# Performance work log

Measured on AMD Instinct MI355X. Metric: run time of the kernel, lower is better.

The kernel has to match this reference:

```python
import jax, jax.numpy as jnp
import numpy as np

B, S, E, H, HD, RD, MP = 2, 2048, 1024, 16, 64, 32, 8  # batch, seq, embed, heads, head_dim, rotary_dim, mp_num


def rotate_every_two(x):
    # x: [..., D] -> interleave (-x_odd, x_even)
    x1 = x[..., ::2]
    x2 = x[..., 1::2]
    return jnp.stack((-x2, x1), axis=-1).reshape(x.shape)


def apply_rotary(x, sin, cos):
    # x: [B,S,H,RD]; sin/cos: [S, RD//2] -> repeat_interleave(2) -> [1,S,1,RD]
    sin = jnp.repeat(sin, 2, axis=-1)[None, :, None, :]
    cos = jnp.repeat(cos, 2, axis=-1)[None, :, None, :]
    return x * cos + rotate_every_two(x) * sin


def setup_inputs() -> dict:
    key = jax.random.key(0)
    k1, k2, k3 = jax.random.split(key, 3)
    return {
        "hidden_states": jax.random.normal(k1, (B, S, E), dtype=jnp.float32),
        "w_qkv": jax.random.normal(k2, (3 * E, E), dtype=jnp.float32) * 0.02,
        "w_out": jax.random.normal(k3, (E, E), dtype=jnp.float32) * 0.02,
    }


def reference(hidden_states, w_qkv, w_out):
    qkv = hidden_states @ w_qkv.T                      # [B,S,3E]
    local = HD * H // MP                               # 128
    qkv = qkv.reshape(B, S, MP, 3 * local)
    # torch.split order in source is (query, value, key)
    q, v, k = jnp.split(qkv, 3, axis=-1)               # each [B,S,MP,local]

    def split_heads(x):
        return x.reshape(B, S, MP, H // MP, HD).reshape(B, S, H, HD)

    q, k, v = split_heads(q), split_heads(k), split_heads(v)  # [B,S,H,HD]

    # fixed sinusoidal rotary embedding over first RD dims
    inv_freq = 1.0 / 10000 ** (jnp.arange(0, RD, 2, dtype=jnp.float32) / RD)
    sinusoid = jnp.arange(S, dtype=jnp.float32)[:, None] * inv_freq[None, :]  # [S, RD//2]
    sin, cos = jnp.sin(sinusoid), jnp.cos(sinusoid)

    q = jnp.concatenate([apply_rotary(q[..., :RD], sin, cos), q[..., RD:]], axis=-1)
    k = jnp.concatenate([apply_rotary(k[..., :RD], sin, cos), k[..., RD:]], axis=-1)

    # [B,H,S,HD]
    q = q.transpose(0, 2, 1, 3)
    k = k.transpose(0, 2, 1, 3)
    v = v.transpose(0, 2, 1, 3)

    scores = jnp.einsum('bhqd,bhkd->bhqk', q, k) / np.float32(np.sqrt(HD))
    causal = jnp.tril(jnp.ones((S, S), dtype=bool))
    scores = jnp.where(causal[None, None], scores, jnp.float32(-1e9))
    attn = jax.nn.softmax(scores.astype(jnp.float32), axis=-1).astype(q.dtype)
    out = jnp.einsum('bhqk,bhkd->bhqd', attn, v)       # [B,H,S,HD]
    out = out.transpose(0, 2, 1, 3).reshape(B, S, E)
    return out @ w_out.T
```

## Files before the change

kernel.cpp:

```cpp
#include <hip/hip_runtime.h>
#include <hip/hip_bf16.h>

typedef __attribute__((ext_vector_type(8))) short short8;
typedef __attribute__((ext_vector_type(4))) float v4f;

#define ASYNC_COPY16(ldsptr, gptr)                                                        \
  __builtin_amdgcn_global_load_lds((const __attribute__((address_space(1))) void*)(gptr), \
                                   (__attribute__((address_space(3))) void*)(ldsptr),     \
                                   16, 0, 0)

__device__ __forceinline__ unsigned short f2bf(float f) {
  unsigned int u = __float_as_uint(f);
  u += 0x7fffu + ((u >> 16) & 1u);
  return (unsigned short)(u >> 16);
}

__global__ void convert_all(const float* __restrict__ h, const float* __restrict__ wq,
                            const float* __restrict__ wo, unsigned short* __restrict__ ho,
                            unsigned short* __restrict__ wqo, unsigned short* __restrict__ woo) {
  int i = (blockIdx.x * blockDim.x + threadIdx.x) * 4;
  const float* src;
  unsigned short* dst;
  int j;
  if (i < 4194304) { src = h; dst = ho; j = i; }
  else if (i < 7340032) { src = wq; dst = wqo; j = i - 4194304; }
  else { src = wo; dst = woo; j = i - 7340032; }
  float4 v = *(const float4*)(src + j);
  ushort4 o;
  o.x = f2bf(v.x); o.y = f2bf(v.y); o.z = f2bf(v.z); o.w = f2bf(v.w);
  *(ushort4*)(dst + j) = o;
}

#define STAGE_SWZ(tt) ((((tt) & 3) ^ (((tt) >> 3) & 3)) * 8)
#define READ_SWZ(kb, lr) (((kb) ^ (((lr) >> 1) & 3)) * 8)

__global__ __launch_bounds__(256, 6) void gemm_out(const unsigned short* __restrict__ A,
                                                   const unsigned short* __restrict__ Bm,
                                                   float* __restrict__ C, int M, int N, int K) {
  __shared__ __attribute__((aligned(16))) unsigned short As[2 * 64 * 32];
  __shared__ __attribute__((aligned(16))) unsigned short Bs[2 * 64 * 32];
  int t = threadIdx.x;
  int w = t >> 6, lane = t & 63, kb = lane >> 4, lr = lane & 15;
  int m0 = blockIdx.y * 64, n0 = blockIdx.x * 64;
  int wm = (w >> 1) * 32, wn = (w & 1) * 32;
  v4f acc[2][2];
#pragma unroll
  for (int i = 0; i < 2; i++)
#pragma unroll
    for (int j = 0; j < 2; j++) acc[i][j] = (v4f){0.f, 0.f, 0.f, 0.f};
  int ra = m0 + (t >> 2);
  int rb = n0 + (t >> 2);
  int ca = STAGE_SWZ(t);
  int rs = READ_SWZ(kb, lr);
  int nit = K >> 5;
  auto stage = [&](int it, int buf) {
    int base = buf * 2048;
    int k0 = it * 32;
    ASYNC_COPY16(&As[base + t * 8], A + (size_t)ra * K + k0 + ca);
    ASYNC_COPY16(&Bs[base + t * 8], Bm + (size_t)rb * K + k0 + ca);
  };
  stage(0, 0);
  __syncthreads();
  for (int it = 0; it < nit; it++) {
    int cur = (it & 1) * 2048;
    if (it + 1 < nit) stage(it + 1, (it + 1) & 1);
    short8 av[2], bv[2];
#pragma unroll
    for (int i = 0; i < 2; i++) av[i] = *(const short8*)&As[cur + (wm + i * 16 + lr) * 32 + rs];
#pragma unroll
    for (int j = 0; j < 2; j++) bv[j] = *(const short8*)&Bs[cur + (wn + j * 16 + lr) * 32 + rs];
#pragma unroll
    for (int i = 0; i < 2; i++)
#pragma unroll
      for (int j = 0; j < 2; j++)
        acc[i][j] = __builtin_amdgcn_mfma_f32_16x16x32_bf16(av[i], bv[j], acc[i][j], 0, 0, 0);
    __syncthreads();
  }
#pragma unroll
  for (int i = 0; i < 2; i++) {
    int row = m0 + wm + i * 16 + kb * 4;
#pragma unroll
    for (int j = 0; j < 2; j++) {
      int col = n0 + wn + j * 16 + lr;
#pragma unroll
      for (int r = 0; r < 4; r++) C[(size_t)(row + r) * N + col] = acc[i][j][r];
    }
  }
}

__global__ __launch_bounds__(256, 6) void gemm_qkv(const unsigned short* __restrict__ A,
                                                   const unsigned short* __restrict__ Bm,
                                                   unsigned short* __restrict__ Q,
                                                   unsigned short* __restrict__ Ko,
                                                   unsigned short* __restrict__ Vt) {
  constexpr int Kd = 1024;
  __shared__ __attribute__((aligned(16))) unsigned short As[2 * 128 * 32];
  __shared__ __attribute__((aligned(16))) unsigned short Bs[2 * 64 * 32];
  int t = threadIdx.x;
  int w = t >> 6, lane = t & 63, kb = lane >> 4, lr = lane & 15;
  int m0 = blockIdx.y * 128, n0 = blockIdx.x * 64;
  int wm = (w >> 1) * 64, wn = (w & 1) * 32;
  v4f acc[4][2];
#pragma unroll
  for (int i = 0; i < 4; i++)
#pragma unroll
    for (int j = 0; j < 2; j++) acc[i][j] = (v4f){0.f, 0.f, 0.f, 0.f};
  int ra = m0 + (t >> 2);
  int rb = n0 + (t >> 2);
  int ca = STAGE_SWZ(t);
  int rs = READ_SWZ(kb, lr);
  auto stage = [&](int it, int buf) {
    int k0 = it * 32;
    int abase = buf * 4096, bbase = buf * 2048;
    ASYNC_COPY16(&As[abase + t * 8],        A + (size_t)ra * Kd + k0 + ca);
    ASYNC_COPY16(&As[abase + 2048 + t * 8], A + (size_t)(ra + 64) * Kd + k0 + ca);
    ASYNC_COPY16(&Bs[bbase + t * 8],        Bm + (size_t)rb * Kd + k0 + ca);
  };
  stage(0, 0);
  __syncthreads();
  for (int it = 0; it < 32; it++) {
    int acur = (it & 1) * 4096, bcur = (it & 1) * 2048;
    if (it + 1 < 32) stage(it + 1, (it + 1) & 1);
    short8 av[4], bv[2];
#pragma unroll
    for (int i = 0; i < 4; i++)
      av[i] = *(const short8*)&As[acur + (wm + i * 16 + lr) * 32 + rs];
#pragma unroll
    for (int j = 0; j < 2; j++)
      bv[j] = *(const short8*)&Bs[bcur + (wn + j * 16 + lr) * 32 + rs];
#pragma unroll
    for (int i = 0; i < 4; i++)
#pragma unroll
      for (int j = 0; j < 2; j++)
        acc[i][j] = __builtin_amdgcn_mfma_f32_16x16x32_bf16(av[i], bv[j], acc[i][j], 0, 0, 0);
    __syncthreads();
  }
  int X = n0 >> 6;
  int mp = X / 6;
  int sub = X - mp * 6;
  int type = sub >> 1;
  int ii = sub & 1;
  int h = mp * 2 + ii;
  const float qs = 0.125f * 1.4426950408889634f;
  if (type == 1) {
#pragma unroll
    for (int i = 0; i < 4; i++) {
      int row = m0 + wm + i * 16 + kb * 4;
#pragma unroll
      for (int j = 0; j < 2; j++) {
        int dim = wn + j * 16 + lr;
#pragma unroll
        for (int r = 0; r < 4; r++) {
          int m = row + r;
          int b = m >> 11, sl = m & 2047;
          int bh = b * 16 + h;
          int p = (sl & ~31) | ((sl & 15) << 1) | ((sl >> 4) & 1);
          Vt[(size_t)bh * 131072 + (size_t)dim * 2048 + p] = f2bf(acc[i][j][r]);
        }
      }
    }
  } else {
    unsigned short* dst = (type == 0) ? Q : Ko;
    float scale = (type == 0) ? qs : 1.0f;
#pragma unroll
    for (int i = 0; i < 4; i++) {
      int row = m0 + wm + i * 16 + kb * 4;
#pragma unroll
      for (int j = 0; j < 2; j++) {
        int dim = wn + j * 16 + lr;
        float vals[4];
#pragma unroll
        for (int r = 0; r < 4; r++) vals[r] = acc[i][j][r];
        if (dim < 32) {
          int jp = dim >> 1;
          float invf = expf(-(float)jp * 0.57564627324851142f);
#pragma unroll
          for (int r = 0; r < 4; r++) {
            int sl = (row + r) & 2047;
            float ang = (float)sl * invf;
            float sn, cs;
            sincosf(ang, &sn, &cs);
            float partner = __shfl_xor(vals[r], 1);
            float self = vals[r] * cs;
            vals[r] = (lr & 1) ? fmaf(partner, sn, self) : fmaf(-partner, sn, self);
          }
        }
#pragma unroll
        for (int r = 0; r < 4; r++) {
          int m = row + r;
          int b = m >> 11, sl = m & 2047;
          int bh = b * 16 + h;
          dst[(((size_t)(bh * 2048 + sl)) << 6) + dim] = f2bf(vals[r] * scale);
        }
      }
    }
  }
}

__global__ __launch_bounds__(256, 6) void attn_fused(const unsigned short* __restrict__ Qg,
                                                     const unsigned short* __restrict__ Kg,
                                                     const unsigned short* __restrict__ Vtg,
                                                     unsigned short* __restrict__ AO,
                                                     float* __restrict__ PO,
                                                     float* __restrict__ PL) {
  __shared__ __attribute__((aligned(16))) unsigned short Ks[2 * 2048];
  __shared__ __attribute__((aligned(16))) unsigned short Vs[2 * 2048];
  __shared__ __attribute__((aligned(16))) unsigned short Ps[4 * 16 * 40];
  int t = threadIdx.x;
  int w = t >> 6, lane = t & 63, kb = lane >> 4, lr = lane & 15;
  int gid = blockIdx.x;
  int g3 = gid & 7;
  int b2 = (gid >> 3) & 3;
  int z = (gid >> 5) & 7;
  int coset = gid >> 8;
  int bh = g3 * 4 + b2;
  int j = (coset == 0) ? (2 * z)
        : (coset == 1) ? (15 - 2 * z)
        : (coset == 2) ? (16 + z)
        : (coset == 3) ? (31 - z)
        : (coset == 4) ? (32 + z)
                       : (47 - z);
  int qtile, kt0, kt1, mode;
  if (j < 16)      { qtile = j;      mode = 0; kt0 = 0;          kt1 = 2 * qtile + 2; }
  else if (j < 32) { qtile = j;      mode = 1; kt0 = 0;          kt1 = qtile + 1; }
  else             { qtile = j - 16; mode = 2; kt0 = qtile + 1;  kt1 = 2 * qtile + 2; }
  int m0 = qtile * 64;
  const unsigned short* Qb = Qg + (size_t)bh * 2048 * 64;
  const unsigned short* Kb = Kg + (size_t)bh * 2048 * 64;
  const unsigned short* Vb = Vtg + (size_t)bh * 64 * 2048;

  short8 aq0 = *(const short8*)(Qb + (size_t)(m0 + w * 16 + lr) * 64 + kb * 8);
  short8 aq1 = *(const short8*)(Qb + (size_t)(m0 + w * 16 + lr) * 64 + 32 + kb * 8);

  v4f acc[4];
  float lp[4];
#pragma unroll
  for (int n = 0; n < 4; n++) acc[n] = (v4f){0.f, 0.f, 0.f, 0.f};
#pragma unroll
  for (int r = 0; r < 4; r++) lp[r] = 0.f;

  int mrow = w * 16 + kb * 4;

  int kc = t >> 5, krow_s = t & 31;
  int vc = t >> 6, vd = t & 63;
  auto stage = [&](int kt, int buf) {
    int base = buf * 2048;
    ASYNC_COPY16(&Ks[base + t * 8], Kb + (size_t)(kt * 32 + krow_s) * 64 + kc * 8);
    ASYNC_COPY16(&Vs[base + t * 8], Vb + (size_t)vd * 2048 + kt * 32 + vc * 8);
  };

  stage(kt0, 0);
  __syncthreads();

  unsigned short* Pw = &Ps[w * 640];
  int niter = kt1 - kt0;
  for (int it = 0; it < niter; it++) {
    int kt = kt0 + it;
    int cur = (it & 1) * 2048;
    if (it + 1 < niter) stage(kt + 1, (it + 1) & 1);
    v4f sc[2];
#pragma unroll
    for (int n2 = 0; n2 < 2; n2++) {
      int krow = n2 * 16 + lr;
      short8 bk0 = *(const short8*)&Ks[cur + (kb * 32 + krow) * 8];
      short8 bk1 = *(const short8*)&Ks[cur + ((kb + 4) * 32 + krow) * 8];
      v4f zz = (v4f){0.f, 0.f, 0.f, 0.f};
      zz = __builtin_amdgcn_mfma_f32_16x16x32_bf16(aq0, bk0, zz, 0, 0, 0);
      zz = __builtin_amdgcn_mfma_f32_16x16x32_bf16(aq1, bk1, zz, 0, 0, 0);
      sc[n2] = zz;
    }
    if (kt >= 2 * qtile) {
#pragma unroll
      for (int n2 = 0; n2 < 2; n2++)
#pragma unroll
        for (int r = 0; r < 4; r++) {
          int key = kt * 32 + n2 * 16 + lr;
          if (key > m0 + mrow + r) sc[n2][r] = -1e30f;
        }
    }
#pragma unroll
    for (int r = 0; r < 4; r++) {
      float p0 = exp2f(sc[0][r]);
      float p1 = exp2f(sc[1][r]);
      lp[r] += p0 + p1;
      __hip_bfloat162 pb = __float22bfloat162_rn(float2{p0, p1});
      *(__hip_bfloat162*)&Pw[(mrow & 15) * 40 + r * 40 + lr * 2] = pb;
    }
    short8 ap = *(const short8*)&Pw[lr * 40 + kb * 8];
#pragma unroll
    for (int dt = 0; dt < 4; dt++) {
      int d = dt * 16 + lr;
      short8 bv = *(const short8*)&Vs[cur + (kb * 64 + d) * 8];
      acc[dt] = __builtin_amdgcn_mfma_f32_16x16x32_bf16(ap, bv, acc[dt], 0, 0, 0);
    }
    __syncthreads();
  }
  float s[4];
#pragma unroll
  for (int r = 0; r < 4; r++) {
    s[r] = lp[r];
#pragma unroll
    for (int off = 1; off < 16; off <<= 1) s[r] += __shfl_xor(s[r], off);
  }
  if (mode == 0) {
    int b = bh >> 4, h = bh & 15;
#pragma unroll
    for (int r = 0; r < 4; r++) {
      float inv = 1.0f / s[r];
      int qrow = m0 + mrow + r;
#pragma unroll
      for (int dt = 0; dt < 4; dt++)
        AO[(size_t)(b * 2048 + qrow) * 1024 + h * 64 + dt * 16 + lr] = f2bf(acc[dt][r] * inv);
    }
  } else {
    int hf = mode - 1;
    size_t pbase = ((size_t)hf * 512 + bh * 16 + (qtile - 16)) * 4096;
    size_t plbase = (size_t)hf * 32768 + (bh * 16 + (qtile - 16)) * 64;
#pragma unroll
    for (int r = 0; r < 4; r++) {
      if (lr == 0) PL[plbase + mrow + r] = s[r];
#pragma unroll
      for (int dt = 0; dt < 4; dt++)
        PO[pbase + (size_t)(mrow + r) * 64 + dt * 16 + lr] = acc[dt][r];
    }
  }
}

__global__ __launch_bounds__(256) void combine(const float* __restrict__ PO,
                                               const float* __restrict__ PL,
                                               unsigned short* __restrict__ AO) {
  int idx = blockIdx.x * 256 + threadIdx.x;
  int d4 = (idx & 15) * 4;
  int row10 = (idx >> 4) & 1023;
  int bh = idx >> 14;
  int q16 = row10 >> 6, lrow = row10 & 63;
  size_t pbase = (((size_t)(bh * 16 + q16)) * 64 + lrow) * 64 + d4;
  float4 a = *(const float4*)&PO[pbase];
  float4 c = *(const float4*)&PO[2097152 + pbase];
  float l = PL[(bh * 16 + q16) * 64 + lrow] + PL[32768 + (bh * 16 + q16) * 64 + lrow];
  float inv = 1.0f / l;
  ushort4 o;
  o.x = f2bf((a.x + c.x) * inv);
  o.y = f2bf((a.y + c.y) * inv);
  o.z = f2bf((a.z + c.z) * inv);
  o.w = f2bf((a.w + c.w) * inv);
  int b = bh >> 4, h = bh & 15;
  int qrow = 1024 + row10;
  *(ushort4*)&AO[(size_t)(b * 2048 + qrow) * 1024 + h * 64 + d4] = o;
}

extern "C" void kernel_launch(void* const* d_in, const int* in_sizes, int n_in,
                              void* d_out, int out_size, void* d_ws, size_t ws_size,
                              hipStream_t stream) {
  const float* hidden = (const float*)d_in[0];
  const float* w_qkv = (const float*)d_in[1];
  const float* w_out = (const float*)d_in[2];
  float* out = (float*)d_out;
  char* ws = (char*)d_ws;
  unsigned short* hid_bf = (unsigned short*)(ws);
  unsigned short* wqkv_bf = (unsigned short*)(ws + (8ull << 20));
  unsigned short* wout_bf = (unsigned short*)(ws + (14ull << 20));
  unsigned short* Qb = (unsigned short*)(ws + (16ull << 20));
  unsigned short* Kb = (unsigned short*)(ws + (24ull << 20));
  unsigned short* Vt = (unsigned short*)(ws + (32ull << 20));
  unsigned short* AO = (unsigned short*)(ws + (40ull << 20));
  float* PO = (float*)(ws + (48ull << 20));
  float* PL = (float*)(ws + (64ull << 20));

  convert_all<<<8192, 256, 0, stream>>>(hidden, w_qkv, w_out, hid_bf, wqkv_bf, wout_bf);
  gemm_qkv<<<dim3(48, 32), 256, 0, stream>>>(hid_bf, wqkv_bf, Qb, Kb, Vt);
  attn_fused<<<1536, 256, 0, stream>>>(Qb, Kb, Vt, AO, PO, PL);
  combine<<<2048, 256, 0, stream>>>(PO, PL, AO);
  gemm_out<<<dim3(16, 64), 256, 0, stream>>>(AO, wout_bf, out, 4096, 1024, 1024);
}
```

Baseline: 192.9 us.

## Fuse fp32-to-bf16 conversion into GEMMs and split-KV combine into output GEMM

Removes the standalone convert kernel: the QKV and output GEMMs now load fp32 operands into registers, convert them to bf16 and store them to LDS, in a register-prefetch / commit pipeline instead of async global-to-LDS copies. The combine kernel is also folded into the output GEMM, which merges the two partial attention outputs and their normalisers while staging the A tile for rows in the second half of the sequence. This drops two launches and the round trips for the bf16 copies and the combined AO, at the cost of reading fp32 weights repeatedly (twice the bytes per tile), higher register pressure, and conversion work on the GEMM critical path.

```diff
diff --git a/kernel.cpp b/kernel.cpp
--- a/kernel.cpp
+++ b/kernel.cpp
@@ -15,81 +15,17 @@
   return (unsigned short)(u >> 16);
 }
 
-__global__ void convert_all(const float* __restrict__ h, const float* __restrict__ wq,
-                            const float* __restrict__ wo, unsigned short* __restrict__ ho,
-                            unsigned short* __restrict__ wqo, unsigned short* __restrict__ woo) {
-  int i = (blockIdx.x * blockDim.x + threadIdx.x) * 4;
-  const float* src;
-  unsigned short* dst;
-  int j;
-  if (i < 4194304) { src = h; dst = ho; j = i; }
-  else if (i < 7340032) { src = wq; dst = wqo; j = i - 4194304; }
-  else { src = wo; dst = woo; j = i - 7340032; }
-  float4 v = *(const float4*)(src + j);
-  ushort4 o;
-  o.x = f2bf(v.x); o.y = f2bf(v.y); o.z = f2bf(v.z); o.w = f2bf(v.w);
-  *(ushort4*)(dst + j) = o;
-}
-
 #define STAGE_SWZ(tt) ((((tt) & 3) ^ (((tt) >> 3) & 3)) * 8)
 #define READ_SWZ(kb, lr) (((kb) ^ (((lr) >> 1) & 3)) * 8)
 
-__global__ __launch_bounds__(256, 6) void gemm_out(const unsigned short* __restrict__ A,
-                                                   const unsigned short* __restrict__ Bm,
-                                                   float* __restrict__ C, int M, int N, int K) {
-  __shared__ __attribute__((aligned(16))) unsigned short As[2 * 64 * 32];
-  __shared__ __attribute__((aligned(16))) unsigned short Bs[2 * 64 * 32];
-  int t = threadIdx.x;
-  int w = t >> 6, lane = t & 63, kb = lane >> 4, lr = lane & 15;
-  int m0 = blockIdx.y * 64, n0 = blockIdx.x * 64;
-  int wm = (w >> 1) * 32, wn = (w & 1) * 32;
-  v4f acc[2][2];
-#pragma unroll
-  for (int i = 0; i < 2; i++)
-#pragma unroll
-    for (int j = 0; j < 2; j++) acc[i][j] = (v4f){0.f, 0.f, 0.f, 0.f};
-  int ra = m0 + (t >> 2);
-  int rb = n0 + (t >> 2);
-  int ca = STAGE_SWZ(t);
-  int rs = READ_SWZ(kb, lr);
-  int nit = K >> 5;
-  auto stage = [&](int it, int buf) {
-    int base = buf * 2048;
-    int k0 = it * 32;
-    ASYNC_COPY16(&As[base + t * 8], A + (size_t)ra * K + k0 + ca);
-    ASYNC_COPY16(&Bs[base + t * 8], Bm + (size_t)rb * K + k0 + ca);
-  };
-  stage(0, 0);
-  __syncthreads();
-  for (int it = 0; it < nit; it++) {
-    int cur = (it & 1) * 2048;
-    if (it + 1 < nit) stage(it + 1, (it + 1) & 1);
-    short8 av[2], bv[2];
-#pragma unroll
-    for (int i = 0; i < 2; i++) av[i] = *(const short8*)&As[cur + (wm + i * 16 + lr) * 32 + rs];
-#pragma unroll
-    for (int j = 0; j < 2; j++) bv[j] = *(const short8*)&Bs[cur + (wn + j * 16 + lr) * 32 + rs];
-#pragma unroll
-    for (int i = 0; i < 2; i++)
-#pragma unroll
-      for (int j = 0; j < 2; j++)
-        acc[i][j] = __builtin_amdgcn_mfma_f32_16x16x32_bf16(av[i], bv[j], acc[i][j], 0, 0, 0);
-    __syncthreads();
-  }
-#pragma unroll
-  for (int i = 0; i < 2; i++) {
-    int row = m0 + wm + i * 16 + kb * 4;
-#pragma unroll
-    for (int j = 0; j < 2; j++) {
-      int col = n0 + wn + j * 16 + lr;
-#pragma unroll
-      for (int r = 0; r < 4; r++) C[(size_t)(row + r) * N + col] = acc[i][j][r];
-    }
-  }
-}
-
-__global__ __launch_bounds__(256, 6) void gemm_qkv(const unsigned short* __restrict__ A,
-                                                   const unsigned short* __restrict__ Bm,
+__device__ __forceinline__ void cvt_store(unsigned short* dst, float4 f0, float4 f1) {
+  unsigned short v8[8] = {f2bf(f0.x), f2bf(f0.y), f2bf(f0.z), f2bf(f0.w),
+                          f2bf(f1.x), f2bf(f1.y), f2bf(f1.z), f2bf(f1.w)};
+  *(short8*)dst = *(short8*)v8;
+}
+
+__global__ __launch_bounds__(256, 5) void gemm_qkv(const float* __restrict__ A,
+                                                   const float* __restrict__ Bm,
                                                    unsigned short* __restrict__ Q,
                                                    unsigned short* __restrict__ Ko,
                                                    unsigned short* __restrict__ Vt) {
@@ -109,18 +45,31 @@
   int rb = n0 + (t >> 2);
   int ca = STAGE_SWZ(t);
   int rs = READ_SWZ(kb, lr);
-  auto stage = [&](int it, int buf) {
+  float4 pa[4], pb[2];
+  auto prefetch = [&](int it) {
     int k0 = it * 32;
+    const float* a0 = A + (size_t)ra * Kd + k0 + ca;
+    const float* a1 = A + (size_t)(ra + 64) * Kd + k0 + ca;
+    const float* b0 = Bm + (size_t)rb * Kd + k0 + ca;
+    pa[0] = *(const float4*)a0;
+    pa[1] = *(const float4*)(a0 + 4);
+    pa[2] = *(const float4*)a1;
+    pa[3] = *(const float4*)(a1 + 4);
+    pb[0] = *(const float4*)b0;
+    pb[1] = *(const float4*)(b0 + 4);
+  };
+  auto commit = [&](int buf) {
     int abase = buf * 4096, bbase = buf * 2048;
-    ASYNC_COPY16(&As[abase + t * 8],        A + (size_t)ra * Kd + k0 + ca);
-    ASYNC_COPY16(&As[abase + 2048 + t * 8], A + (size_t)(ra + 64) * Kd + k0 + ca);
-    ASYNC_COPY16(&Bs[bbase + t * 8],        Bm + (size_t)rb * Kd + k0 + ca);
-  };
-  stage(0, 0);
+    cvt_store(&As[abase + t * 8], pa[0], pa[1]);
+    cvt_store(&As[abase + 2048 + t * 8], pa[2], pa[3]);
+    cvt_store(&Bs[bbase + t * 8], pb[0], pb[1]);
+  };
+  prefetch(0);
+  commit(0);
   __syncthreads();
   for (int it = 0; it < 32; it++) {
     int acur = (it & 1) * 4096, bcur = (it & 1) * 2048;
-    if (it + 1 < 32) stage(it + 1, (it + 1) & 1);
+    if (it < 31) prefetch(it + 1);
     short8 av[4], bv[2];
 #pragma unroll
     for (int i = 0; i < 4; i++)
@@ -133,6 +82,7 @@
 #pragma unroll
       for (int j = 0; j < 2; j++)
         acc[i][j] = __builtin_amdgcn_mfma_f32_16x16x32_bf16(av[i], bv[j], acc[i][j], 0, 0, 0);
+    if (it < 31) commit((it + 1) & 1);
     __syncthreads();
   }
   int X = n0 >> 6;
@@ -326,27 +276,91 @@
   }
 }
 
-__global__ __launch_bounds__(256) void combine(const float* __restrict__ PO,
-                                               const float* __restrict__ PL,
-                                               unsigned short* __restrict__ AO) {
-  int idx = blockIdx.x * 256 + threadIdx.x;
-  int d4 = (idx & 15) * 4;
-  int row10 = (idx >> 4) & 1023;
-  int bh = idx >> 14;
-  int q16 = row10 >> 6, lrow = row10 & 63;
-  size_t pbase = (((size_t)(bh * 16 + q16)) * 64 + lrow) * 64 + d4;
-  float4 a = *(const float4*)&PO[pbase];
-  float4 c = *(const float4*)&PO[2097152 + pbase];
-  float l = PL[(bh * 16 + q16) * 64 + lrow] + PL[32768 + (bh * 16 + q16) * 64 + lrow];
-  float inv = 1.0f / l;
-  ushort4 o;
-  o.x = f2bf((a.x + c.x) * inv);
-  o.y = f2bf((a.y + c.y) * inv);
-  o.z = f2bf((a.z + c.z) * inv);
-  o.w = f2bf((a.w + c.w) * inv);
-  int b = bh >> 4, h = bh & 15;
-  int qrow = 1024 + row10;
-  *(ushort4*)&AO[(size_t)(b * 2048 + qrow) * 1024 + h * 64 + d4] = o;
+__global__ __launch_bounds__(256, 4) void gemm_out(const unsigned short* __restrict__ AO,
+                                                   const float* __restrict__ PO,
+                                                   const float* __restrict__ PL,
+                                                   const float* __restrict__ Bm,
+                                                   float* __restrict__ C) {
+  constexpr int Kd = 1024, Nd = 1024;
+  __shared__ __attribute__((aligned(16))) unsigned short As[2 * 64 * 32];
+  __shared__ __attribute__((aligned(16))) unsigned short Bs[2 * 64 * 32];
+  int t = threadIdx.x;
+  int w = t >> 6, lane = t & 63, kb = lane >> 4, lr = lane & 15;
+  int m0 = blockIdx.y * 64, n0 = blockIdx.x * 64;
+  bool comb = (blockIdx.y >> 4) & 1;
+  int wm = (w >> 1) * 32, wn = (w & 1) * 32;
+  v4f acc[2][2];
+#pragma unroll
+  for (int i = 0; i < 2; i++)
+#pragma unroll
+    for (int j = 0; j < 2; j++) acc[i][j] = (v4f){0.f, 0.f, 0.f, 0.f};
+  int ra = m0 + (t >> 2);
+  int rb = n0 + (t >> 2);
+  int ca = STAGE_SWZ(t);
+  int rs = READ_SWZ(kb, lr);
+  int b = ra >> 11, qrow = ra & 2047;
+  int q16 = (qrow >> 6) - 16, lrow = qrow & 63;
+  float4 pb[2], pa0[2], pa1[2];
+  float lsum = 1.0f;
+  auto prefetch = [&](int it, int buf) {
+    int k0 = it * 32;
+    const float* b0 = Bm + (size_t)rb * Kd + k0 + ca;
+    pb[0] = *(const float4*)b0;
+    pb[1] = *(const float4*)(b0 + 4);
+    if (comb) {
+      int h = k0 >> 6, d0 = (k0 & 32) + ca;
+      size_t idx = ((size_t)((b * 16 + h) * 16 + q16) * 64 + lrow) * 64 + d0;
+      pa0[0] = *(const float4*)&PO[idx];
+      pa0[1] = *(const float4*)&PO[idx + 4];
+      pa1[0] = *(const float4*)&PO[2097152 + idx];
+      pa1[1] = *(const float4*)&PO[2097152 + idx + 4];
+      int pli = ((b * 16 + h) * 16 + q16) * 64 + lrow;
+      lsum = PL[pli] + PL[32768 + pli];
+    } else {
+      ASYNC_COPY16(&As[buf * 2048 + t * 8], AO + (size_t)ra * Kd + k0 + ca);
+    }
+  };
+  auto commit = [&](int buf) {
+    cvt_store(&Bs[buf * 2048 + t * 8], pb[0], pb[1]);
+    if (comb) {
+      float inv = 1.0f / lsum;
+      float4 f0, f1;
+      f0.x = (pa0[0].x + pa1[0].x) * inv; f0.y = (pa0[0].y + pa1[0].y) * inv;
+      f0.z = (pa0[0].z + pa1[0].z) * inv; f0.w = (pa0[0].w + pa1[0].w) * inv;
+      f1.x = (pa0[1].x + pa1[1].x) * inv; f1.y = (pa0[1].y + pa1[1].y) * inv;
+      f1.z = (pa0[1].z + pa1[1].z) * inv; f1.w = (pa0[1].w + pa1[1].w) * inv;
+      cvt_store(&As[buf * 2048 + t * 8], f0, f1);
+    }
+  };
+  prefetch(0, 0);
+  commit(0);
+  __syncthreads();
+  for (int it = 0; it < 32; it++) {
+    int cur = (it & 1) * 2048;
+    if (it < 31) prefetch(it + 1, (it + 1) & 1);
+    short8 av[2], bv[2];
+#pragma unroll
+    for (int i = 0; i < 2; i++) av[i] = *(const short8*)&As[cur + (wm + i * 16 + lr) * 32 + rs];
+#pragma unroll
+    for (int j = 0; j < 2; j++) bv[j] = *(const short8*)&Bs[cur + (wn + j * 16 + lr) * 32 + rs];
+#pragma unroll
+    for (int i = 0; i < 2; i++)
+#pragma unroll
+      for (int j = 0; j < 2; j++)
+        acc[i][j] = __builtin_amdgcn_mfma_f32_16x16x32_bf16(av[i], bv[j], acc[i][j], 0, 0, 0);
+    if (it < 31) commit((it + 1) & 1);
+    __syncthreads();
+  }
+#pragma unroll
+  for (int i = 0; i < 2; i++) {
+    int row = m0 + wm + i * 16 + kb * 4;
+#pragma unroll
+    for (int j = 0; j < 2; j++) {
+      int col = n0 + wn + j * 16 + lr;
+#pragma unroll
+      for (int r = 0; r < 4; r++) C[(size_t)(row + r) * Nd + col] = acc[i][j][r];
+    }
+  }
 }
 
 extern "C" void kernel_launch(void* const* d_in, const int* in_sizes, int n_in,
@@ -357,9 +371,6 @@
   const float* w_out = (const float*)d_in[2];
   float* out = (float*)d_out;
   char* ws = (char*)d_ws;
-  unsigned short* hid_bf = (unsigned short*)(ws);
-  unsigned short* wqkv_bf = (unsigned short*)(ws + (8ull << 20));
-  unsigned short* wout_bf = (unsigned short*)(ws + (14ull << 20));
   unsigned short* Qb = (unsigned short*)(ws + (16ull << 20));
   unsigned short* Kb = (unsigned short*)(ws + (24ull << 20));
   unsigned short* Vt = (unsigned short*)(ws + (32ull << 20));
@@ -367,9 +378,7 @@
   float* PO = (float*)(ws + (48ull << 20));
   float* PL = (float*)(ws + (64ull << 20));
 
-  convert_all<<<8192, 256, 0, stream>>>(hidden, w_qkv, w_out, hid_bf, wqkv_bf, wout_bf);
-  gemm_qkv<<<dim3(48, 32), 256, 0, stream>>>(hid_bf, wqkv_bf, Qb, Kb, Vt);
+  gemm_qkv<<<dim3(48, 32), 256, 0, stream>>>(hidden, w_qkv, Qb, Kb, Vt);
   attn_fused<<<1536, 256, 0, stream>>>(Qb, Kb, Vt, AO, PO, PL);
-  combine<<<2048, 256, 0, stream>>>(PO, PL, AO);
-  gemm_out<<<dim3(16, 64), 256, 0, stream>>>(AO, wout_bf, out, 4096, 1024, 1024);
-}
+  gemm_out<<<dim3(16, 64), 256, 0, stream>>>(AO, PO, PL, w_out, out);
+}
```

Result: slower. 222.0 us (+15.1%).
